# Kernel optimization log

Measured on AMD Instinct MI355X. Metric: run time of the kernel, lower is better.

Reference implementation:

```python
import jax, jax.numpy as jnp
import numpy as np

B, T, H, L, O = 4096, 128, 156, 2, 12  # batch, input_len, nodes/hidden, num_layers, output_len


def setup_inputs() -> dict:
    key = jax.random.key(0)
    ks = jax.random.split(key, 24)
    s = 0.05
    mat = lambda k: jax.random.normal(k, (L, H, H), jnp.float32) * s
    vec = lambda k: jax.random.normal(k, (L, H), jnp.float32) * s
    return {
        "x": jax.random.normal(ks[0], (B, T, H), jnp.float32),
        "adj": jax.random.uniform(ks[1], (H, H), jnp.float32) / H,  # row-normalized-ish adjacency
        "Wix": mat(ks[2]), "bix": vec(ks[3]),
        "Wih": mat(ks[4]), "bih": vec(ks[5]),
        "Wfx": mat(ks[6]), "bfx": vec(ks[7]),
        "Wfh": mat(ks[8]), "bfh": vec(ks[9]),
        "Wcx": mat(ks[10]), "bcx": vec(ks[11]),
        "Wch": mat(ks[12]), "bch": vec(ks[13]),
        "Wox": mat(ks[14]), "box": vec(ks[15]),
        "Woh": mat(ks[16]), "boh": vec(ks[17]),
        "gcn_w1": jax.random.normal(ks[18], (L,), jnp.float32),  # GraphConvolution 1x1 weights
        "gcn_w2": jax.random.normal(ks[19], (L,), jnp.float32),
        "W_out": jax.random.normal(ks[20], (O, T), jnp.float32) * s,
        "b_out": jnp.zeros((O,), jnp.float32),
    }


def _gcn(state, adj, w1, w2):
    # batched version of the per-sample GCN: state [B,H] -> columns X [H,B]
    X = state.T
    h1 = jax.nn.relu((adj @ X) * w1)        # layer1: mm(adj,x) @ 1x1 weight, relu
    h2 = jax.nn.sigmoid((adj @ h1) * w2)    # layer2: same, sigmoid
    return h2.T                              # back to [B,H]


def reference(x, adj, Wix, bix, Wih, bih, Wfx, bfx, Wfh, bfh,
              Wcx, bcx, Wch, bch, Wox, box, Woh, boh,
              gcn_w1, gcn_w2, W_out, b_out):
    Bsz, Tlen, F = x.shape
    Ln = Wix.shape[0]
    cs0 = jnp.zeros((Ln, Bsz, F), x.dtype)
    hs0 = jnp.zeros((Ln, Bsz, F), x.dtype)

    def step(carry, inp):
        cs, hs = carry
        x_t, i = inp  # x_t: [B,F]; every layer consumes the raw input (as in the torch code)
        first = (i == 0)
        new_c, new_h = [], []
        ht = None
        for j in range(Ln):
            c, h = cs[j], hs[j]
            cg = _gcn(c, adj, gcn_w1[j], gcn_w2[j])
            hg = _gcn(h, adj, gcn_w1[j], gcn_w2[j])
            c = jnp.where(first, c, cg)  # GCN applied only for t > 0
            h = jnp.where(first, h, hg)
            it = jax.nn.sigmoid(x_t @ Wix[j].T + bix[j] + h @ Wih[j].T + bih[j])
            ft = jax.nn.sigmoid(x_t @ Wfx[j].T + bfx[j] + h @ Wfh[j].T + bfh[j])
            ot = jax.nn.sigmoid(x_t @ Wox[j].T + box[j] + h @ Woh[j].T + boh[j])
            ct = ft * c + it * jnp.tanh(x_t @ Wcx[j].T + bcx[j] + h @ Wch[j].T + bch[j])
            ht = ot * jnp.tanh(ct)
            new_c.append(ct)
            new_h.append(ht)
        return (jnp.stack(new_c), jnp.stack(new_h)), ht

    (c_n, h_n), ys = jax.lax.scan(
        step, (cs0, hs0), (jnp.swapaxes(x, 0, 1), jnp.arange(Tlen)))
    out = jnp.swapaxes(ys, 0, 1)            # [B,T,F]
    out = out.reshape(Bsz, F, Tlen)         # torch .view(B,-1,T) on contiguous [B,T,F]
    out = out @ W_out.T + b_out             # hidden2out over time dim -> [B,F,O]
    out = out.reshape(Bsz, W_out.shape[0], F)  # torch .view(B,O,-1)
    return out, h_n, c_n
```

## Files before the change

kernel.cpp:

```cpp
#include <hip/hip_runtime.h>


#define HH 156
#define HP 160
#define TT 128
#define OO 12
#define BB 32
#define LDSS 168
#define MATSZ 25600

typedef _Float16 f16x8 __attribute__((ext_vector_type(8)));
typedef _Float16 f16x4 __attribute__((ext_vector_type(4)));
typedef float    f32x4 __attribute__((ext_vector_type(4)));

__device__ __forceinline__ float sigm(float v) { return 1.0f / (1.0f + __expf(-v)); }
__device__ __forceinline__ float tanh_(float v) { return 2.0f / (1.0f + __expf(-2.0f * v)) - 1.0f; }

__global__ __launch_bounds__(256) void prep_kernel(
    const float* __restrict__ adj,
    const float* __restrict__ Wix, const float* __restrict__ Wih,
    const float* __restrict__ Wfx, const float* __restrict__ Wfh,
    const float* __restrict__ Wcx, const float* __restrict__ Wch,
    const float* __restrict__ Wox, const float* __restrict__ Woh,
    const float* __restrict__ bix, const float* __restrict__ bih,
    const float* __restrict__ bfx, const float* __restrict__ bfh,
    const float* __restrict__ bcx, const float* __restrict__ bch,
    const float* __restrict__ box_, const float* __restrict__ boh,
    _Float16* __restrict__ wmats, float* __restrict__ bias_comb)
{
    int idx = blockIdx.x * 256 + threadIdx.x;
    if (idx < 17 * MATSZ) {
        int mat = idx / MATSZ;
        int r   = idx % MATSZ;
        int e    = r & 7;
        int lane = (r >> 3) & 63;
        int c    = r >> 9;
        int lcol = lane & 15, quad = lane >> 4;
        int kk = c % 5, w = c / 5;
        int nrow = w * 16 + lcol;
        int k    = kk * 32 + quad * 8 + e;
        float v = 0.f;
        if (nrow < HH && k < HH) {
            if (mat == 0) {
                v = adj[nrow * HH + k];
            } else {
                int m2 = mat - 1;
                int s  = m2 & 1;
                int jg = m2 >> 1;
                int j  = jg >> 2;
                int g  = jg & 3;
                const float* W;
                if (s == 0) W = (g == 0) ? Wix : (g == 1) ? Wfx : (g == 2) ? Wox : Wcx;
                else        W = (g == 0) ? Wih : (g == 1) ? Wfh : (g == 2) ? Woh : Wch;
                v = W[j * (HH * HH) + nrow * HH + k];
            }
        }
        wmats[idx] = (_Float16)v;
    } else if (idx < 17 * MATSZ + 2 * 4 * HP) {
        int r = idx - 17 * MATSZ;
        int j = r / (4 * HP);
        int g = (r % (4 * HP)) / HP;
        int nn = r % HP;
        float v = 0.f;
        if (nn < HH) {
            const float* Bx = (g == 0) ? bix : (g == 1) ? bfx : (g == 2) ? box_ : bcx;
            const float* Bh = (g == 0) ? bih : (g == 1) ? bfh : (g == 2) ? boh : bch;
            v = Bx[j * HH + nn] + Bh[j * HH + nn];
        }
        bias_comb[r] = v;
    }
}

__device__ __forceinline__ void dma16(const _Float16* g, _Float16* l) {
    __builtin_amdgcn_global_load_lds(
        (const __attribute__((address_space(1))) void*)(g),
        (__attribute__((address_space(3))) void*)(l), 16, 0, 0);
}

__device__ __forceinline__ void stage_mat(_Float16* buf, const _Float16* gmat,
                                          int wave, int lane) {
    #pragma unroll
    for (int i = 0; i < 5; ++i) {
        const int c = wave * 5 + i;
        dma16(gmat + (size_t)c * 512 + lane * 8, buf + (size_t)c * 512);
    }
}

__global__ __launch_bounds__(640, 3) void lstm_main(
    const float* __restrict__ x,
    const _Float16* __restrict__ wmats,
    const float* __restrict__ bias_comb,
    const float* __restrict__ w_out,
    const float* __restrict__ b_out,
    const float* __restrict__ gcn_w1,
    const float* __restrict__ gcn_w2,
    float* __restrict__ out)
{
    __shared__ __align__(16) _Float16 st_c[BB][LDSS];
    __shared__ __align__(16) _Float16 st_h[BB][LDSS];
    __shared__ __align__(16) _Float16 tmp[BB][LDSS];
    __shared__ __align__(16) _Float16 xb[BB][LDSS];
    __shared__ __align__(16) _Float16 wout_s[OO][TT + 8];
    extern __shared__ __align__(16) _Float16 wbuf[];

    const int tid   = threadIdx.x;
    const int wave  = tid >> 6;
    const int lane  = tid & 63;
    const int lcol  = lane & 15;
    const int quad  = lane >> 4;
    const int qoff  = quad << 3;
    const int layer = blockIdx.x & 1;
    const int b0    = (blockIdx.x >> 1) << 5;
    const int n     = (wave << 4) + lcol;

    for (int e = tid; e < BB * LDSS; e += 640) {
        (&st_c[0][0])[e] = (_Float16)0.f;
        (&st_h[0][0])[e] = (_Float16)0.f;
        (&xb[0][0])[e]   = (_Float16)0.f;
    }
    for (int e = tid; e < OO * TT; e += 640) wout_s[e / TT][e % TT] = (_Float16)w_out[e];

    float bias_r[4];
    #pragma unroll
    for (int g = 0; g < 4; ++g)
        bias_r[g] = bias_comb[(layer * 4 + g) * HP + n];
    const float gw1 = gcn_w1[layer];
    const float gw2 = gcn_w2[layer];
    const float bout_r = (lcol < OO) ? b_out[lcol] : 0.f;

    f16x8 badj[5];
    #pragma unroll
    for (int kk = 0; kk < 5; ++kk)
        badj[kk] = *(const f16x8*)&wmats[((size_t)(wave * 5 + kk) * 64 + lane) * 8];

    const _Float16* gw = wmats + (size_t)(1 + layer * 8) * MATSZ;
    __syncthreads();

    f32x4 pacc = {0.f, 0.f, 0.f, 0.f};
    int cur_i = wave >> 1;
    const int pmt = wave & 1;

    auto proj_step = [&](int tp) {
        if (cur_i > HH - 1) return;
        const int s = cur_i * TT - tp * HH;
        if (s > HH - 1) return;
        const int lc = (lcol < OO) ? lcol : 0;
        #pragma unroll
        for (int kk = 0; kk < 5; ++kk) {
            f16x8 b;
            #pragma unroll
            for (int e = 0; e < 8; ++e) {
                int f  = kk * 32 + qoff + e;
                int tq = f - s;
                bool ok = (lcol < OO) && (tq >= 0) && (tq < TT) && (f < HH);
                int tqc = tq < 0 ? 0 : (tq > TT - 1 ? TT - 1 : tq);
                b[e] = ok ? wout_s[lc][tqc] : (_Float16)0.f;
            }
            f16x8 a = *(const f16x8*)&st_h[pmt * 16 + lcol][kk * 32 + qoff];
            pacc = __builtin_amdgcn_mfma_f32_16x16x32_f16(a, b, pacc, 0, 0, 0);
        }
        if (s <= 28) {
            if (lcol < OO) {
                #pragma unroll
                for (int r = 0; r < 4; ++r)
                    out[(size_t)(b0 + pmt * 16 + (quad << 2) + r) * (HH * OO)
                        + cur_i * OO + lcol] = pacc[r] + bout_r;
            }
            pacc = (f32x4){0.f, 0.f, 0.f, 0.f};
            cur_i += 3;
        }
    };

    for (int t = 0; t < TT; ++t) {
        float4 vx[5];
        if (wave >= 6) {
            const int e0 = tid - 384;
            #pragma unroll
            for (int it = 0; it < 5; ++it) {
                int e = e0 + it * 256;
                int m = e / 40, q = e % 40, f = q << 2;
                float4 v = make_float4(0.f, 0.f, 0.f, 0.f);
                if (f + 4 <= HH) v = *(const float4*)&x[((size_t)(b0 + m) * TT + t) * HH + f];
                vx[it] = v;
            }
        }
        stage_mat(wbuf,          gw,          wave, lane);
        stage_mat(wbuf + MATSZ,  gw + MATSZ,  wave, lane);

        if (wave >= 6) {
            const int e0 = tid - 384;
            #pragma unroll
            for (int it = 0; it < 5; ++it) {
                int e = e0 + it * 256;
                int m = e / 40, q = e % 40, f = q << 2;
                f16x4 h4 = {(_Float16)vx[it].x, (_Float16)vx[it].y,
                            (_Float16)vx[it].z, (_Float16)vx[it].w};
                *(f16x4*)&xb[m][f] = h4;
            }
        } else if (layer && t > 0) {
            proj_step(t - 1);
        }
        __syncthreads();

        if (t > 0) {
            #pragma unroll
            for (int S = 0; S < 2; ++S) {
                const _Float16* Ab = S ? &st_h[0][0] : &st_c[0][0];
                #pragma unroll
                for (int mt = 0; mt < 2; ++mt) {
                    f32x4 acc = {0.f, 0.f, 0.f, 0.f};
                    #pragma unroll
                    for (int kk = 0; kk < 5; ++kk) {
                        f16x8 a = *(const f16x8*)&Ab[(size_t)(mt * 16 + lcol) * LDSS + kk * 32 + qoff];
                        acc = __builtin_amdgcn_mfma_f32_16x16x32_f16(a, badj[kk], acc, 0, 0, 0);
                    }
                    #pragma unroll
                    for (int r = 0; r < 4; ++r) {
                        float v = acc[r] * gw1;
                        tmp[mt * 16 + (quad << 2) + r][n] = (_Float16)(v > 0.f ? v : 0.f);
                    }
                }
                __syncthreads();
                _Float16 (*dst)[LDSS] = S ? st_h : st_c;
                #pragma unroll
                for (int mt = 0; mt < 2; ++mt) {
                    f32x4 acc = {0.f, 0.f, 0.f, 0.f};
                    #pragma unroll
                    for (int kk = 0; kk < 5; ++kk) {
                        f16x8 a = *(const f16x8*)&tmp[mt * 16 + lcol][kk * 32 + qoff];
                        acc = __builtin_amdgcn_mfma_f32_16x16x32_f16(a, badj[kk], acc, 0, 0, 0);
                    }
                    #pragma unroll
                    for (int r = 0; r < 4; ++r)
                        dst[mt * 16 + (quad << 2) + r][n] = (_Float16)sigm(acc[r] * gw2);
                }
                __syncthreads();
            }
        }

        f32x4 acc[8];
        #pragma unroll
        for (int a2 = 0; a2 < 8; ++a2) acc[a2] = (f32x4){0.f, 0.f, 0.f, 0.f};
        #pragma unroll
        for (int m = 0; m < 8; ++m) {
            if (m < 7) asm volatile("s_waitcnt vmcnt(5)" ::: "memory");
            else       asm volatile("s_waitcnt vmcnt(0)" ::: "memory");
            __builtin_amdgcn_sched_barrier(0);
            const _Float16* wbc = wbuf + (size_t)(m & 1) * MATSZ;
            f16x8 bw[5];
            #pragma unroll
            for (int kk = 0; kk < 5; ++kk)
                bw[kk] = *(const f16x8*)&wbc[((size_t)(wave * 5 + kk) * 64 + lane) * 8];
            const _Float16* Ab = (m & 1) ? &st_h[0][0] : &xb[0][0];
            const int g = m >> 1;
            #pragma unroll
            for (int mt = 0; mt < 2; ++mt) {
                #pragma unroll
                for (int kk = 0; kk < 5; ++kk) {
                    f16x8 a = *(const f16x8*)&Ab[(size_t)(mt * 16 + lcol) * LDSS + kk * 32 + qoff];
                    acc[g * 2 + mt] = __builtin_amdgcn_mfma_f32_16x16x32_f16(
                        a, bw[kk], acc[g * 2 + mt], 0, 0, 0);
                }
            }
            __builtin_amdgcn_sched_barrier(0);
            if (m + 2 < 8)
                stage_mat(wbuf + (size_t)(m & 1) * MATSZ, gw + (size_t)(m + 2) * MATSZ,
                          wave, lane);
        }
        __syncthreads();

        #pragma unroll
        for (int mt = 0; mt < 2; ++mt) {
            #pragma unroll
            for (int r = 0; r < 4; ++r) {
                int m = mt * 16 + (quad << 2) + r;
                float i_ = sigm(acc[0 * 2 + mt][r] + bias_r[0]);
                float f_ = sigm(acc[1 * 2 + mt][r] + bias_r[1]);
                float o_ = sigm(acc[2 * 2 + mt][r] + bias_r[2]);
                float g_ = tanh_(acc[3 * 2 + mt][r] + bias_r[3]);
                float c_old = (float)st_c[m][n];
                float c_new = f_ * c_old + i_ * g_;
                float h_new = o_ * tanh_(c_new);
                st_c[m][n] = (_Float16)c_new;
                st_h[m][n] = (_Float16)h_new;
            }
        }
        __syncthreads();
    }

    if (layer && wave < 6) proj_step(TT - 1);

    float* hn = out + (size_t)4096 * HH * OO;
    float* cn = hn + (size_t)2 * 4096 * HH;
    for (int e = tid; e < BB * HH; e += 640) {
        int m = e / HH;
        int f = e % HH;
        size_t off = ((size_t)layer * 4096 + b0 + m) * HH + f;
        hn[off] = (float)st_h[m][f];
        cn[off] = (float)st_c[m][f];
    }
}

extern "C" void kernel_launch(void* const* d_in, const int* in_sizes, int n_in,
                              void* d_out, int out_size, void* d_ws, size_t ws_size,
                              hipStream_t stream) {
    const float* x    = (const float*)d_in[0];
    const float* adj  = (const float*)d_in[1];
    const float* Wix  = (const float*)d_in[2];  const float* bix = (const float*)d_in[3];
    const float* Wih  = (const float*)d_in[4];  const float* bih = (const float*)d_in[5];
    const float* Wfx  = (const float*)d_in[6];  const float* bfx = (const float*)d_in[7];
    const float* Wfh  = (const float*)d_in[8];  const float* bfh = (const float*)d_in[9];
    const float* Wcx  = (const float*)d_in[10]; const float* bcx = (const float*)d_in[11];
    const float* Wch  = (const float*)d_in[12]; const float* bch = (const float*)d_in[13];
    const float* Wox  = (const float*)d_in[14]; const float* box_ = (const float*)d_in[15];
    const float* Woh  = (const float*)d_in[16]; const float* boh = (const float*)d_in[17];
    const float* gw1  = (const float*)d_in[18];
    const float* gw2  = (const float*)d_in[19];
    const float* Wout = (const float*)d_in[20];
    const float* bout = (const float*)d_in[21];

    _Float16* wmats   = (_Float16*)d_ws;
    float* bias_comb  = (float*)((char*)d_ws + (size_t)17 * MATSZ * sizeof(_Float16));
    float* out        = (float*)d_out;

    prep_kernel<<<(17 * MATSZ + 2 * 4 * HP + 255) / 256, 256, 0, stream>>>(
        adj, Wix, Wih, Wfx, Wfh, Wcx, Wch, Wox, Woh,
        bix, bih, bfx, bfh, bcx, bch, box_, boh, wmats, bias_comb);

    (void)hipFuncSetAttribute((const void*)lstm_main,
                              hipFuncAttributeMaxDynamicSharedMemorySize,
                              2 * MATSZ * sizeof(_Float16));

    lstm_main<<<256, 640, 2 * MATSZ * sizeof(_Float16), stream>>>(
        x, wmats, bias_comb, Wout, bout, gw1, gw2, out);
}
```

Measured before the change: 2.430 ms.

## Use fragment-major LDS layout, merge GCN passes, and prefetch next-step weights

Replaces the row-major padded LDS tiles with a layout ordered by MFMA fragment, so A-operand loads become contiguous per-lane 16-byte reads. The c and h GCN passes are merged so each layer needs two barriers instead of four. The GCN result for c is kept in registers, and the x/h fragments are preloaded into registers before the gate GEMMs. Staging of the first two weight matrices for the next timestep is moved to right after the gate GEMMs so it overlaps the elementwise LSTM update. It also adds lighter LDS-only barriers. One risk: the xbf padding columns are no longer zeroed, so uninitialized LDS could feed the MFMAs.

```diff
diff --git a/kernel.cpp b/kernel.cpp
--- a/kernel.cpp
+++ b/kernel.cpp
@@ -6,8 +6,8 @@
 #define TT 128
 #define OO 12
 #define BB 32
-#define LDSS 168
 #define MATSZ 25600
+#define FMAT  5120
 
 typedef _Float16 f16x8 __attribute__((ext_vector_type(8)));
 typedef _Float16 f16x4 __attribute__((ext_vector_type(4)));
@@ -15,6 +15,10 @@
 
 __device__ __forceinline__ float sigm(float v) { return 1.0f / (1.0f + __expf(-v)); }
 __device__ __forceinline__ float tanh_(float v) { return 2.0f / (1.0f + __expf(-2.0f * v)) - 1.0f; }
+
+#define LBAR() do { asm volatile("s_waitcnt lgkmcnt(0)" ::: "memory"); \
+                    __builtin_amdgcn_s_barrier();                      \
+                    __builtin_amdgcn_sched_barrier(0); } while (0)
 
 __global__ __launch_bounds__(256) void prep_kernel(
     const float* __restrict__ adj,
@@ -86,6 +90,10 @@
     }
 }
 
+__device__ __forceinline__ int fidx(int m, int k) {
+    return (((m >> 4) * 5 + (k >> 5)) * 64 + ((k >> 3) & 3) * 16 + (m & 15)) * 8 + (k & 7);
+}
+
 __global__ __launch_bounds__(640, 3) void lstm_main(
     const float* __restrict__ x,
     const _Float16* __restrict__ wmats,
@@ -96,10 +104,10 @@
     const float* __restrict__ gcn_w2,
     float* __restrict__ out)
 {
-    __shared__ __align__(16) _Float16 st_c[BB][LDSS];
-    __shared__ __align__(16) _Float16 st_h[BB][LDSS];
-    __shared__ __align__(16) _Float16 tmp[BB][LDSS];
-    __shared__ __align__(16) _Float16 xb[BB][LDSS];
+    __shared__ __align__(16) _Float16 st_c[FMAT];
+    __shared__ __align__(16) _Float16 st_h[FMAT];
+    __shared__ __align__(16) _Float16 tmpf[2][FMAT];
+    __shared__ __align__(16) _Float16 xbf[FMAT];
     __shared__ __align__(16) _Float16 wout_s[OO][TT + 8];
     extern __shared__ __align__(16) _Float16 wbuf[];
 
@@ -112,11 +120,11 @@
     const int layer = blockIdx.x & 1;
     const int b0    = (blockIdx.x >> 1) << 5;
     const int n     = (wave << 4) + lcol;
-
-    for (int e = tid; e < BB * LDSS; e += 640) {
-        (&st_c[0][0])[e] = (_Float16)0.f;
-        (&st_h[0][0])[e] = (_Float16)0.f;
-        (&xb[0][0])[e]   = (_Float16)0.f;
+    const int colb  = ((n >> 5) * 64 + ((n >> 3) & 3) * 16) * 8 + (n & 7);
+
+    for (int e = tid; e < FMAT; e += 640) {
+        st_c[e] = (_Float16)0.f;
+        st_h[e] = (_Float16)0.f;
     }
     for (int e = tid; e < OO * TT; e += 640) wout_s[e / TT][e % TT] = (_Float16)w_out[e];
 
@@ -133,8 +141,11 @@
     for (int kk = 0; kk < 5; ++kk)
         badj[kk] = *(const f16x8*)&wmats[((size_t)(wave * 5 + kk) * 64 + lane) * 8];
 
-    const _Float16* gw = wmats + (size_t)(1 + layer * 8) * MATSZ;
+    const _Float16* gwp = wmats + (size_t)(1 + layer * 8) * MATSZ;
     __syncthreads();
+
+    stage_mat(wbuf,         gwp,         wave, lane);
+    stage_mat(wbuf + MATSZ, gwp + MATSZ, wave, lane);
 
     f32x4 pacc = {0.f, 0.f, 0.f, 0.f};
     int cur_i = wave >> 1;
@@ -156,7 +167,7 @@
                 int tqc = tq < 0 ? 0 : (tq > TT - 1 ? TT - 1 : tq);
                 b[e] = ok ? wout_s[lc][tqc] : (_Float16)0.f;
             }
-            f16x8 a = *(const f16x8*)&st_h[pmt * 16 + lcol][kk * 32 + qoff];
+            f16x8 a = *(const f16x8*)&st_h[((pmt * 5 + kk) * 64 + lane) * 8];
             pacc = __builtin_amdgcn_mfma_f32_16x16x32_f16(a, b, pacc, 0, 0, 0);
         }
         if (s <= 28) {
@@ -171,10 +182,12 @@
         }
     };
 
+    float cgr[2][4];
+
     for (int t = 0; t < TT; ++t) {
-        float4 vx[5];
         if (wave >= 6) {
             const int e0 = tid - 384;
+            float4 vx[5];
             #pragma unroll
             for (int it = 0; it < 5; ++it) {
                 int e = e0 + it * 256;
@@ -183,109 +196,129 @@
                 if (f + 4 <= HH) v = *(const float4*)&x[((size_t)(b0 + m) * TT + t) * HH + f];
                 vx[it] = v;
             }
-        }
-        stage_mat(wbuf,          gw,          wave, lane);
-        stage_mat(wbuf + MATSZ,  gw + MATSZ,  wave, lane);
-
-        if (wave >= 6) {
-            const int e0 = tid - 384;
             #pragma unroll
             for (int it = 0; it < 5; ++it) {
                 int e = e0 + it * 256;
                 int m = e / 40, q = e % 40, f = q << 2;
                 f16x4 h4 = {(_Float16)vx[it].x, (_Float16)vx[it].y,
                             (_Float16)vx[it].z, (_Float16)vx[it].w};
-                *(f16x4*)&xb[m][f] = h4;
+                *(f16x4*)&xbf[fidx(m, f)] = h4;
             }
         } else if (layer && t > 0) {
             proj_step(t - 1);
         }
-        __syncthreads();
 
         if (t > 0) {
             #pragma unroll
             for (int S = 0; S < 2; ++S) {
-                const _Float16* Ab = S ? &st_h[0][0] : &st_c[0][0];
+                const _Float16* Ab = S ? st_h : st_c;
                 #pragma unroll
                 for (int mt = 0; mt < 2; ++mt) {
-                    f32x4 acc = {0.f, 0.f, 0.f, 0.f};
+                    f32x4 a1 = {0.f, 0.f, 0.f, 0.f};
                     #pragma unroll
                     for (int kk = 0; kk < 5; ++kk) {
-                        f16x8 a = *(const f16x8*)&Ab[(size_t)(mt * 16 + lcol) * LDSS + kk * 32 + qoff];
-                        acc = __builtin_amdgcn_mfma_f32_16x16x32_f16(a, badj[kk], acc, 0, 0, 0);
+                        f16x8 a = *(const f16x8*)&Ab[((mt * 5 + kk) * 64 + lane) * 8];
+                        a1 = __builtin_amdgcn_mfma_f32_16x16x32_f16(a, badj[kk], a1, 0, 0, 0);
                     }
                     #pragma unroll
                     for (int r = 0; r < 4; ++r) {
-                        float v = acc[r] * gw1;
-                        tmp[mt * 16 + (quad << 2) + r][n] = (_Float16)(v > 0.f ? v : 0.f);
+                        float v = a1[r] * gw1;
+                        tmpf[S][mt * 2560 + colb + ((quad << 2) + r) * 8] =
+                            (_Float16)(v > 0.f ? v : 0.f);
                     }
                 }
-                __syncthreads();
-                _Float16 (*dst)[LDSS] = S ? st_h : st_c;
-                #pragma unroll
-                for (int mt = 0; mt < 2; ++mt) {
-                    f32x4 acc = {0.f, 0.f, 0.f, 0.f};
-                    #pragma unroll
-                    for (int kk = 0; kk < 5; ++kk) {
-                        f16x8 a = *(const f16x8*)&tmp[mt * 16 + lcol][kk * 32 + qoff];
-                        acc = __builtin_amdgcn_mfma_f32_16x16x32_f16(a, badj[kk], acc, 0, 0, 0);
-                    }
-                    #pragma unroll
-                    for (int r = 0; r < 4; ++r)
-                        dst[mt * 16 + (quad << 2) + r][n] = (_Float16)sigm(acc[r] * gw2);
+            }
+        }
+        LBAR();
+
+        if (t > 0) {
+            #pragma unroll
+            for (int mt = 0; mt < 2; ++mt) {
+                f32x4 a0 = {0.f, 0.f, 0.f, 0.f}, a1 = {0.f, 0.f, 0.f, 0.f};
+                #pragma unroll
+                for (int kk = 0; kk < 5; ++kk) {
+                    f16x8 ac = *(const f16x8*)&tmpf[0][((mt * 5 + kk) * 64 + lane) * 8];
+                    f16x8 ahh = *(const f16x8*)&tmpf[1][((mt * 5 + kk) * 64 + lane) * 8];
+                    a0 = __builtin_amdgcn_mfma_f32_16x16x32_f16(ac, badj[kk], a0, 0, 0, 0);
+                    a1 = __builtin_amdgcn_mfma_f32_16x16x32_f16(ahh, badj[kk], a1, 0, 0, 0);
                 }
-                __syncthreads();
-            }
-        }
+                #pragma unroll
+                for (int r = 0; r < 4; ++r) {
+                    cgr[mt][r] = (float)(_Float16)sigm(a0[r] * gw2);
+                    st_h[mt * 2560 + colb + ((quad << 2) + r) * 8] =
+                        (_Float16)sigm(a1[r] * gw2);
+                }
+            }
+        } else {
+            #pragma unroll
+            for (int mt = 0; mt < 2; ++mt)
+                #pragma unroll
+                for (int r = 0; r < 4; ++r) cgr[mt][r] = 0.f;
+        }
+        LBAR();
+
+        f16x8 ax[2][5], ah[2][5];
+        #pragma unroll
+        for (int mt = 0; mt < 2; ++mt)
+            #pragma unroll
+            for (int kk = 0; kk < 5; ++kk) {
+                ax[mt][kk] = *(const f16x8*)&xbf[((mt * 5 + kk) * 64 + lane) * 8];
+                ah[mt][kk] = *(const f16x8*)&st_h[((mt * 5 + kk) * 64 + lane) * 8];
+            }
 
         f32x4 acc[8];
         #pragma unroll
         for (int a2 = 0; a2 < 8; ++a2) acc[a2] = (f32x4){0.f, 0.f, 0.f, 0.f};
         #pragma unroll
         for (int m = 0; m < 8; ++m) {
-            if (m < 7) asm volatile("s_waitcnt vmcnt(5)" ::: "memory");
-            else       asm volatile("s_waitcnt vmcnt(0)" ::: "memory");
+            if (m == 0 || m == 7) asm volatile("s_waitcnt vmcnt(0)" ::: "memory");
+            else                  asm volatile("s_waitcnt vmcnt(5)" ::: "memory");
             __builtin_amdgcn_sched_barrier(0);
             const _Float16* wbc = wbuf + (size_t)(m & 1) * MATSZ;
             f16x8 bw[5];
             #pragma unroll
             for (int kk = 0; kk < 5; ++kk)
                 bw[kk] = *(const f16x8*)&wbc[((size_t)(wave * 5 + kk) * 64 + lane) * 8];
-            const _Float16* Ab = (m & 1) ? &st_h[0][0] : &xb[0][0];
             const int g = m >> 1;
             #pragma unroll
             for (int mt = 0; mt < 2; ++mt) {
                 #pragma unroll
                 for (int kk = 0; kk < 5; ++kk) {
-                    f16x8 a = *(const f16x8*)&Ab[(size_t)(mt * 16 + lcol) * LDSS + kk * 32 + qoff];
+                    f16x8 a = (m & 1) ? ah[mt][kk] : ax[mt][kk];
                     acc[g * 2 + mt] = __builtin_amdgcn_mfma_f32_16x16x32_f16(
                         a, bw[kk], acc[g * 2 + mt], 0, 0, 0);
                 }
             }
-            __builtin_amdgcn_sched_barrier(0);
-            if (m + 2 < 8)
-                stage_mat(wbuf + (size_t)(m & 1) * MATSZ, gw + (size_t)(m + 2) * MATSZ,
+            if (m < 6) {
+                asm volatile("s_waitcnt lgkmcnt(0)" ::: "memory");
+                __builtin_amdgcn_sched_barrier(0);
+                stage_mat(wbuf + (size_t)(m & 1) * MATSZ, gwp + (size_t)(m + 2) * MATSZ,
                           wave, lane);
-        }
-        __syncthreads();
+            }
+        }
+        LBAR();
+
+        if (t + 1 < TT) {
+            stage_mat(wbuf,         gwp,         wave, lane);
+            stage_mat(wbuf + MATSZ, gwp + MATSZ, wave, lane);
+        }
 
         #pragma unroll
         for (int mt = 0; mt < 2; ++mt) {
             #pragma unroll
             for (int r = 0; r < 4; ++r) {
-                int m = mt * 16 + (quad << 2) + r;
                 float i_ = sigm(acc[0 * 2 + mt][r] + bias_r[0]);
                 float f_ = sigm(acc[1 * 2 + mt][r] + bias_r[1]);
                 float o_ = sigm(acc[2 * 2 + mt][r] + bias_r[2]);
                 float g_ = tanh_(acc[3 * 2 + mt][r] + bias_r[3]);
-                float c_old = (float)st_c[m][n];
-                float c_new = f_ * c_old + i_ * g_;
+                float c_new = f_ * cgr[mt][r] + i_ * g_;
                 float h_new = o_ * tanh_(c_new);
-                st_c[m][n] = (_Float16)c_new;
-                st_h[m][n] = (_Float16)h_new;
-            }
-        }
-        __syncthreads();
+                const int fi = mt * 2560 + colb + ((quad << 2) + r) * 8;
+                st_c[fi] = (_Float16)c_new;
+                st_h[fi] = (_Float16)h_new;
+            }
+        }
+        LBAR();
     }
 
     if (layer && wave < 6) proj_step(TT - 1);
@@ -296,8 +329,9 @@
         int m = e / HH;
         int f = e % HH;
         size_t off = ((size_t)layer * 4096 + b0 + m) * HH + f;
-        hn[off] = (float)st_h[m][f];
-        cn[off] = (float)st_c[m][f];
+        int fi = fidx(m, f);
+        hn[off] = (float)st_h[fi];
+        cn[off] = (float)st_c[fi];
     }
 }
 
```

Measured after the change: 3.528 ms. 1.45x slower.
